# Optimization experiments

Measured on AMD Instinct MI355X. Metric: run time of the kernel, lower is better.

Reference implementation:

```python
import jax, jax.numpy as jnp
import numpy as np

B, S, E, H = 2, 2048, 1024, 16
D = E // H  # head_dim = 64


def setup_inputs() -> dict:
    key = jax.random.key(0)
    k1, k2, k3 = jax.random.split(key, 3)
    scale_in = 1.0 / np.sqrt(E)
    return {
        "x": jax.random.normal(k1, (B, S, E), dtype=jnp.float32),
        "W_attn": jax.random.normal(k2, (E, 3 * E), dtype=jnp.float32) * scale_in,
        "b_attn": jnp.zeros((3 * E,), dtype=jnp.float32),
        "W_proj": jax.random.normal(k3, (E, E), dtype=jnp.float32) * scale_in,
        "b_proj": jnp.zeros((E,), dtype=jnp.float32),
    }


def reference(x, W_attn, b_attn, W_proj, b_proj):
    # c_attn: fused QKV projection  [B,S,E] -> [B,S,3E]
    qkv = x @ W_attn + b_attn
    q, k, v = jnp.split(qkv, 3, axis=-1)
    # split heads -> [B,S,H,D]
    q = q.reshape(B, S, H, D)
    k = k.reshape(B, S, H, D)
    v = v.reshape(B, S, H, D)
    # scaled dot-product attention (no causal mask in the source module)
    scores = jnp.einsum("bqhd,bkhd->bhqk", q, k) / jnp.sqrt(jnp.float32(D))
    attn = jax.nn.softmax(scores, axis=-1)  # attn_dropout is identity in eval
    y = jnp.einsum("bhqk,bkhd->bqhd", attn, v).reshape(B, S, E)
    # c_proj; resid_dropout is identity in eval
    return y @ W_proj + b_proj
```

## Files before the change

kernel.cpp:

```cpp
#include <hip/hip_runtime.h>
#include <stdint.h>

#define NB 2
#define NS 2048
#define NE 1024
#define NH 16
#define ND 64
#define NE3 3072
#define NBS 4096
#define NT 32

typedef _Float16 half8 __attribute__((ext_vector_type(8)));
typedef __fp16 fp16x2 __attribute__((ext_vector_type(2)));
typedef float f32x4 __attribute__((ext_vector_type(4)));
typedef float f32x16 __attribute__((ext_vector_type(16)));
typedef unsigned int u32;

__device__ __forceinline__ void gload16(const void* g, void* l) {
  __builtin_amdgcn_global_load_lds(
      (__attribute__((address_space(1))) void*)const_cast<void*>(g),
      (__attribute__((address_space(3))) void*)l, 16, 0, 0);
}

__global__ void k_cvt16(const float* __restrict__ src, _Float16* __restrict__ dst, int n8) {
  int i = blockIdx.x * blockDim.x + threadIdx.x;
  if (i >= n8) return;
  const float4* s = (const float4*)src + (size_t)i * 2;
  float4 a = s[0], b = s[1];
  half8 o;
  o[0]=(_Float16)a.x; o[1]=(_Float16)a.y; o[2]=(_Float16)a.z; o[3]=(_Float16)a.w;
  o[4]=(_Float16)b.x; o[5]=(_Float16)b.y; o[6]=(_Float16)b.z; o[7]=(_Float16)b.w;
  *((half8*)dst + i) = o;
}

__global__ void k_cvtT(const float* __restrict__ src, _Float16* __restrict__ dst, int K, int N) {
  __shared__ _Float16 tile[64][72];
  int n0 = blockIdx.x * 64, k0 = blockIdx.y * 64;
  int t = threadIdx.x;
  int kk = t >> 2, nc = (t & 3) << 4;
  const float* sp = src + (size_t)(k0 + kk) * N + n0 + nc;
#pragma unroll
  for (int j = 0; j < 16; j += 4) {
    float4 v = *(const float4*)(sp + j);
    tile[kk][nc + j + 0] = (_Float16)v.x;
    tile[kk][nc + j + 1] = (_Float16)v.y;
    tile[kk][nc + j + 2] = (_Float16)v.z;
    tile[kk][nc + j + 3] = (_Float16)v.w;
  }
  __syncthreads();
  int nn = t >> 2, kc = (t & 3) << 4;
  half8 o0, o1;
#pragma unroll
  for (int j = 0; j < 8; ++j) { o0[j] = tile[kc + j][nn]; o1[j] = tile[kc + 8 + j][nn]; }
  _Float16* op = dst + (size_t)(n0 + nn) * K + k0 + kc;
  *(half8*)op = o0;
  *(half8*)(op + 8) = o1;
}

template <int OUT_HALF>
__global__ __launch_bounds__(256, 2)
void k_gemm(const _Float16* __restrict__ A, const _Float16* __restrict__ Bt,
            const float* __restrict__ bias, void* __restrict__ Cv,
            int M, int N, int K) {
  __shared__ _Float16 As[128 * 32];
  __shared__ _Float16 Bs[128 * 32];
  const int nwg = gridDim.x * gridDim.y;
  const int d = blockIdx.y * gridDim.x + blockIdx.x;
  const int lid = (d & 7) * (nwg >> 3) + (d >> 3);
  const int bx = lid % gridDim.x, by = lid / gridDim.x;
  const int m0 = by * 128, n0 = bx * 128;
  const int t = threadIdx.x, l = t & 63, w = t >> 6;
  const int wr = w >> 1, wc = w & 1;
  const int srow = l >> 2;
  const int sk = (l & 3) << 3;
  f32x4 acc[4][4] = {};
  for (int kt = 0; kt < K; kt += 32) {
    __syncthreads();
#pragma unroll
    for (int i = 0; i < 2; ++i) {
      int rb = (i * 4 + w) * 16;
      gload16(A + (size_t)(m0 + rb + srow) * K + kt + sk, (char*)As + (i * 4 + w) * 1024);
      gload16(Bt + (size_t)(n0 + rb + srow) * K + kt + sk, (char*)Bs + (i * 4 + w) * 1024);
    }
    __syncthreads();
    half8 a[4], b[4];
#pragma unroll
    for (int i = 0; i < 4; ++i)
      a[i] = *(const half8*)(As + (wr * 64 + i * 16 + (l & 15)) * 32 + ((l >> 4) << 3));
#pragma unroll
    for (int j = 0; j < 4; ++j)
      b[j] = *(const half8*)(Bs + (wc * 64 + j * 16 + (l & 15)) * 32 + ((l >> 4) << 3));
#pragma unroll
    for (int i = 0; i < 4; ++i)
#pragma unroll
      for (int j = 0; j < 4; ++j)
        acc[i][j] = __builtin_amdgcn_mfma_f32_16x16x32_f16(a[i], b[j], acc[i][j], 0, 0, 0);
  }
  float bv[4];
#pragma unroll
  for (int j = 0; j < 4; ++j) bv[j] = bias[n0 + wc * 64 + j * 16 + (l & 15)];
#pragma unroll
  for (int i = 0; i < 4; ++i) {
    int row0 = m0 + wr * 64 + i * 16 + ((l >> 4) << 2);
#pragma unroll
    for (int j = 0; j < 4; ++j) {
      int col = n0 + wc * 64 + j * 16 + (l & 15);
#pragma unroll
      for (int r = 0; r < 4; ++r) {
        float v = acc[i][j][r] + bv[j];
        if (OUT_HALF && col < NE) v *= 0.18033688011112042f;
        if (OUT_HALF)
          ((_Float16*)Cv)[(size_t)(row0 + r) * N + col] = (_Float16)v;
        else
          ((float*)Cv)[(size_t)(row0 + r) * N + col] = v;
      }
    }
  }
}

__global__ void k_vt(const _Float16* __restrict__ qkv, _Float16* __restrict__ Vt) {
  __shared__ _Float16 tile[64][72];
  int s0 = blockIdx.x * 64;
  int bh = blockIdx.y, b = bh >> 4, h = bh & 15;
  int t = threadIdx.x;
  int ss = t >> 2, dc = (t & 3) << 4;
  const _Float16* sp = qkv + (size_t)(b * NS + s0 + ss) * NE3 + 2 * NE + h * ND + dc;
  half8 v0 = *(const half8*)sp, v1 = *(const half8*)(sp + 8);
#pragma unroll
  for (int j = 0; j < 8; ++j) { tile[ss][dc + j] = v0[j]; tile[ss][dc + 8 + j] = v1[j]; }
  __syncthreads();
  int d = t >> 2, sc = (t & 3) << 4;
  half8 o0, o1;
#pragma unroll
  for (int j = 0; j < 8; ++j) { o0[j] = tile[sc + j][d]; o1[j] = tile[sc + 8 + j][d]; }
  _Float16* op = Vt + (size_t)(bh * ND + d) * NS + s0 + sc;
  *(half8*)op = o0;
  *(half8*)(op + 8) = o1;
}

__global__ __launch_bounds__(256, 2)
void k_attn(const _Float16* __restrict__ qkv, const _Float16* __restrict__ Vt,
            _Float16* __restrict__ Y) {
  __shared__ _Float16 Kb[2][64 * 64];
  __shared__ _Float16 Vb[2][64 * 64];
  const int dly = blockIdx.y * gridDim.x + blockIdx.x;
  const int lid = (dly & 7) * 64 + (dly >> 3);
  const int bh = lid >> 4, qb = lid & 15;
  const int q0 = qb * 128;
  const int b = bh >> 4, h = bh & 15;
  const int t = threadIdx.x, l = t & 63, w = t >> 6;
  const int c = l & 31, hh = l >> 5;

  half8 qf[4];
  {
    const _Float16* qp = qkv + (size_t)(b * NS + q0 + w * 32 + c) * NE3 + h * ND + 8 * hh;
    qf[0] = *(const half8*)(qp);
    qf[1] = *(const half8*)(qp + 16);
    qf[2] = *(const half8*)(qp + 32);
    qf[3] = *(const half8*)(qp + 48);
  }

  f32x16 Oa0 = {}, Oa1 = {}, Osum = {};
  f32x16 saE0, saE1, saO0, saO1;
  half8 ones;
#pragma unroll
  for (int j = 0; j < 8; ++j) ones[j] = (_Float16)1.0f;

  const int lh4 = l >> 4;
  const int ls7 = (l >> 1) & 7;
  const int l1 = l & 1;
  const int grp = c >> 1;
  const int xr = grp & 7;

#define RD_BASE (grp * 256 + ((c & 1) << 4))

#define STAGE_K(KT, BUF)                                                             \
  {                                                                                  \
    _Pragma("unroll")                                                                \
    for (int i = 0; i < 2; ++i) {                                                    \
      int ci = w * 2 + i;                                                            \
      int g = 4 * ci + lh4;                                                          \
      int row = 2 * g + l1;                                                          \
      int j8 = (ls7 ^ (g & 7)) << 3;                                                 \
      gload16(qkv + (size_t)(b * NS + (KT) * 64 + row) * NE3 + NE + h * ND + j8,     \
              (char*)&Kb[BUF][0] + ci * 1024);                                       \
    }                                                                                \
  }
#define STAGE_V(KT, BUF)                                                             \
  {                                                                                  \
    _Pragma("unroll")                                                                \
    for (int i = 0; i < 2; ++i) {                                                    \
      int ci = w * 2 + i;                                                            \
      int g = 4 * ci + lh4;                                                          \
      int row = 2 * g + l1;                                                          \
      int j8 = (ls7 ^ (g & 7)) << 3;                                                 \
      gload16(Vt + (size_t)(bh * ND + row) * NS + (KT) * 64 + j8,                    \
              (char*)&Vb[BUF][0] + ci * 1024);                                       \
    }                                                                                \
  }

#define QK_TILE(BUF, SA0, SA1)                                                       \
  {                                                                                  \
    SA0 = (f32x16){}; SA1 = (f32x16){};                                              \
    _Pragma("unroll")                                                                \
    for (int tt = 0; tt < 4; ++tt) {                                                 \
      int off = RD_BASE + (((2 * tt + hh) ^ xr) << 5);                               \
      half8 kf0 = *(const half8*)((char*)&Kb[BUF][0] + off);                         \
      half8 kf1 = *(const half8*)((char*)&Kb[BUF][0] + off + 4096);                  \
      SA0 = __builtin_amdgcn_mfma_f32_32x32x16_f16(kf0, qf[tt], SA0, 0, 0, 0);       \
      SA1 = __builtin_amdgcn_mfma_f32_32x32x16_f16(kf1, qf[tt], SA1, 0, 0, 0);       \
    }                                                                                \
  }

#define PVSTEP(KK, DARR, CUR)                                                         \
    {                                                                                 \
      u32 pb0 = DARR[2 * ((KK) & 1)][0], pa0 = DARR[2 * ((KK) & 1) + 1][0];           \
      u32 pb1 = DARR[2 * ((KK) & 1)][1], pa1 = DARR[2 * ((KK) & 1) + 1][1];           \
      u32 sent0 = hh ? pb0 : pa0;                                                     \
      u32 sent1 = hh ? pb1 : pa1;                                                     \
      u32 recv0 = __shfl_xor(sent0, 32);                                              \
      u32 recv1 = __shfl_xor(sent1, 32);                                              \
      union { u32 d[4]; half8 h; } pfu;                                               \
      pfu.d[0] = hh ? recv0 : pb0;                                                    \
      pfu.d[1] = hh ? recv1 : pb1;                                                    \
      pfu.d[2] = hh ? pa0 : recv0;                                                    \
      pfu.d[3] = hh ? pa1 : recv1;                                                    \
      int offv = RD_BASE + (((2 * (KK) + hh) ^ xr) << 5);                             \
      half8 vf0 = *(const half8*)((char*)&Vb[CUR][0] + offv);                         \
      half8 vf1 = *(const half8*)((char*)&Vb[CUR][0] + offv + 4096);                  \
      Oa0 = __builtin_amdgcn_mfma_f32_32x32x16_f16(pfu.h, vf0, Oa0, 0, 0, 0);         \
      Oa1 = __builtin_amdgcn_mfma_f32_32x32x16_f16(pfu.h, vf1, Oa1, 0, 0, 0);         \
      Osum = __builtin_amdgcn_mfma_f32_32x32x16_f16(pfu.h, ones, Osum, 0, 0, 0);      \
    }

#define TILE_BODY(T, CUR, SAC0, SAC1, SAN0, SAN1)                                     \
  {                                                                                   \
    u32 D0[4][2], D1[4][2];                                                           \
    _Pragma("unroll")                                                                 \
    for (int s = 0; s < 4; ++s) {                                                     \
      fp16x2 e0 = __builtin_amdgcn_cvt_pkrtz(__builtin_amdgcn_exp2f(SAC0[4 * s + 0]), \
                                             __builtin_amdgcn_exp2f(SAC0[4 * s + 1]));\
      fp16x2 e1 = __builtin_amdgcn_cvt_pkrtz(__builtin_amdgcn_exp2f(SAC0[4 * s + 2]), \
                                             __builtin_amdgcn_exp2f(SAC0[4 * s + 3]));\
      fp16x2 e2 = __builtin_amdgcn_cvt_pkrtz(__builtin_amdgcn_exp2f(SAC1[4 * s + 0]), \
                                             __builtin_amdgcn_exp2f(SAC1[4 * s + 1]));\
      fp16x2 e3 = __builtin_amdgcn_cvt_pkrtz(__builtin_amdgcn_exp2f(SAC1[4 * s + 2]), \
                                             __builtin_amdgcn_exp2f(SAC1[4 * s + 3]));\
      D0[s][0] = __builtin_bit_cast(u32, e0);                                         \
      D0[s][1] = __builtin_bit_cast(u32, e1);                                         \
      D1[s][0] = __builtin_bit_cast(u32, e2);                                         \
      D1[s][1] = __builtin_bit_cast(u32, e3);                                         \
    }                                                                                 \
    if ((T) + 1 < NT) QK_TILE((CUR) ^ 1, SAN0, SAN1);                                 \
    PVSTEP(0, D0, CUR)                                                                \
    PVSTEP(1, D0, CUR)                                                                \
    PVSTEP(2, D1, CUR)                                                                \
    PVSTEP(3, D1, CUR)                                                                \
    __syncthreads();                                                                  \
    if ((T) + 2 < NT) STAGE_V((T) + 2, CUR);                                          \
    if ((T) + 3 < NT) STAGE_K((T) + 3, (CUR) ^ 1);                                    \
  }

  STAGE_K(0, 0);
  STAGE_V(0, 0);
  STAGE_K(1, 1);
  __syncthreads();
  QK_TILE(0, saE0, saE1);
  __syncthreads();
  STAGE_V(1, 1);
  STAGE_K(2, 0);

  for (int kt = 0; kt < NT; kt += 2) {
    TILE_BODY(kt, 0, saE0, saE1, saO0, saO1);
    TILE_BODY(kt + 1, 1, saO0, saO1, saE0, saE1);
  }
#undef TILE_BODY
#undef PVSTEP
#undef QK_TILE
#undef STAGE_K
#undef STAGE_V
#undef RD_BASE

#pragma unroll
  for (int i = 0; i < 16; ++i) {
    int ql = (i & 3) + 8 * (i >> 2) + 4 * hh;
    float inv = 1.0f / Osum[i];
    size_t base = (size_t)(b * NS + q0 + w * 32 + ql) * NE + h * ND + c;
    Y[base] = (_Float16)(Oa0[i] * inv);
    Y[base + 32] = (_Float16)(Oa1[i] * inv);
  }
}

extern "C" void kernel_launch(void* const* d_in, const int* in_sizes, int n_in,
                              void* d_out, int out_size, void* d_ws, size_t ws_size,
                              hipStream_t stream) {
  (void)in_sizes; (void)n_in; (void)out_size; (void)ws_size;
  const float* x      = (const float*)d_in[0];
  const float* W_attn = (const float*)d_in[1];
  const float* b_attn = (const float*)d_in[2];
  const float* W_proj = (const float*)d_in[3];
  const float* b_proj = (const float*)d_in[4];
  char* ws = (char*)d_ws;
  const size_t MB = 1024 * 1024;
  _Float16* qkvb = (_Float16*)(ws);
  _Float16* WaT  = (_Float16*)(ws + 24 * MB);
  _Float16* WpT  = (_Float16*)(ws + 30 * MB);
  _Float16* xb   = (_Float16*)(ws + 32 * MB);
  _Float16* Vt   = (_Float16*)(ws + 40 * MB);
  _Float16* yb   = (_Float16*)(ws + 32 * MB);

  k_cvt16<<<dim3(2048), dim3(256), 0, stream>>>(x, xb, NBS * NE / 8);
  k_cvtT<<<dim3(48, 16), dim3(256), 0, stream>>>(W_attn, WaT, NE, NE3);
  k_cvtT<<<dim3(16, 16), dim3(256), 0, stream>>>(W_proj, WpT, NE, NE);
  k_gemm<1><<<dim3(NE3 / 128, NBS / 128), dim3(256), 0, stream>>>(xb, WaT, b_attn, (void*)qkvb, NBS, NE3, NE);
  k_vt<<<dim3(NS / 64, NB * NH), dim3(256), 0, stream>>>(qkvb, Vt);
  k_attn<<<dim3(NS / 128, NB * NH), dim3(256), 0, stream>>>(qkvb, Vt, yb);
  k_gemm<0><<<dim3(NE / 128, NBS / 128), dim3(256), 0, stream>>>(yb, WpT, b_proj, d_out, NBS, NE, NE);
}
```

Baseline: 129.2 us.

## Fuse V transpose into QKV GEMM epilogue and raise MFMA wave priority

The QKV GEMM epilogue now writes the V columns straight into the transposed Vt layout, so the separate k_vt transpose kernel and its launch are removed. In the attention kernel, s_setprio brackets the MFMA sequences to favour matrix-issuing waves. The transposed stores are strided per element, roughly 4 KB apart for adjacent rows, so they coalesce poorly and may slow the GEMM epilogue.

```diff
diff --git a/kernel.cpp b/kernel.cpp
--- a/kernel.cpp
+++ b/kernel.cpp
@@ -61,7 +61,7 @@
 __global__ __launch_bounds__(256, 2)
 void k_gemm(const _Float16* __restrict__ A, const _Float16* __restrict__ Bt,
             const float* __restrict__ bias, void* __restrict__ Cv,
-            int M, int N, int K) {
+            _Float16* __restrict__ VtOut, int M, int N, int K) {
   __shared__ _Float16 As[128 * 32];
   __shared__ _Float16 Bs[128 * 32];
   const int nwg = gridDim.x * gridDim.y;
@@ -108,34 +108,22 @@
 #pragma unroll
       for (int r = 0; r < 4; ++r) {
         float v = acc[i][j][r] + bv[j];
-        if (OUT_HALF && col < NE) v *= 0.18033688011112042f;
-        if (OUT_HALF)
-          ((_Float16*)Cv)[(size_t)(row0 + r) * N + col] = (_Float16)v;
-        else
-          ((float*)Cv)[(size_t)(row0 + r) * N + col] = v;
+        int row = row0 + r;
+        if (OUT_HALF) {
+          if (col < NE) v *= 0.18033688011112042f;
+          if (col >= 2 * NE) {
+            int vcol = col - 2 * NE;
+            int bb = row >> 11, ss = row & (NS - 1);
+            VtOut[(size_t)((bb << 10) + vcol) * NS + ss] = (_Float16)v;
+          } else {
+            ((_Float16*)Cv)[(size_t)row * N + col] = (_Float16)v;
+          }
+        } else {
+          ((float*)Cv)[(size_t)row * N + col] = v;
+        }
       }
     }
   }
-}
-
-__global__ void k_vt(const _Float16* __restrict__ qkv, _Float16* __restrict__ Vt) {
-  __shared__ _Float16 tile[64][72];
-  int s0 = blockIdx.x * 64;
-  int bh = blockIdx.y, b = bh >> 4, h = bh & 15;
-  int t = threadIdx.x;
-  int ss = t >> 2, dc = (t & 3) << 4;
-  const _Float16* sp = qkv + (size_t)(b * NS + s0 + ss) * NE3 + 2 * NE + h * ND + dc;
-  half8 v0 = *(const half8*)sp, v1 = *(const half8*)(sp + 8);
-#pragma unroll
-  for (int j = 0; j < 8; ++j) { tile[ss][dc + j] = v0[j]; tile[ss][dc + 8 + j] = v1[j]; }
-  __syncthreads();
-  int d = t >> 2, sc = (t & 3) << 4;
-  half8 o0, o1;
-#pragma unroll
-  for (int j = 0; j < 8; ++j) { o0[j] = tile[sc + j][d]; o1[j] = tile[sc + 8 + j][d]; }
-  _Float16* op = Vt + (size_t)(bh * ND + d) * NS + s0 + sc;
-  *(half8*)op = o0;
-  *(half8*)(op + 8) = o1;
 }
 
 __global__ __launch_bounds__(256, 2)
@@ -202,6 +190,7 @@
 #define QK_TILE(BUF, SA0, SA1)                                                       \
   {                                                                                  \
     SA0 = (f32x16){}; SA1 = (f32x16){};                                              \
+    __builtin_amdgcn_s_setprio(1);                                                   \
     _Pragma("unroll")                                                                \
     for (int tt = 0; tt < 4; ++tt) {                                                 \
       int off = RD_BASE + (((2 * tt + hh) ^ xr) << 5);                               \
@@ -210,6 +199,7 @@
       SA0 = __builtin_amdgcn_mfma_f32_32x32x16_f16(kf0, qf[tt], SA0, 0, 0, 0);       \
       SA1 = __builtin_amdgcn_mfma_f32_32x32x16_f16(kf1, qf[tt], SA1, 0, 0, 0);       \
     }                                                                                \
+    __builtin_amdgcn_s_setprio(0);                                                   \
   }
 
 #define PVSTEP(KK, DARR, CUR)                                                         \
@@ -228,9 +218,11 @@
       int offv = RD_BASE + (((2 * (KK) + hh) ^ xr) << 5);                             \
       half8 vf0 = *(const half8*)((char*)&Vb[CUR][0] + offv);                         \
       half8 vf1 = *(const half8*)((char*)&Vb[CUR][0] + offv + 4096);                  \
+      __builtin_amdgcn_s_setprio(1);                                                  \
       Oa0 = __builtin_amdgcn_mfma_f32_32x32x16_f16(pfu.h, vf0, Oa0, 0, 0, 0);         \
       Oa1 = __builtin_amdgcn_mfma_f32_32x32x16_f16(pfu.h, vf1, Oa1, 0, 0, 0);         \
       Osum = __builtin_amdgcn_mfma_f32_32x32x16_f16(pfu.h, ones, Osum, 0, 0, 0);      \
+      __builtin_amdgcn_s_setprio(0);                                                  \
     }
 
 #define TILE_BODY(T, CUR, SAC0, SAC1, SAN0, SAN1)                                     \
@@ -312,8 +304,7 @@
   k_cvt16<<<dim3(2048), dim3(256), 0, stream>>>(x, xb, NBS * NE / 8);
   k_cvtT<<<dim3(48, 16), dim3(256), 0, stream>>>(W_attn, WaT, NE, NE3);
   k_cvtT<<<dim3(16, 16), dim3(256), 0, stream>>>(W_proj, WpT, NE, NE);
-  k_gemm<1><<<dim3(NE3 / 128, NBS / 128), dim3(256), 0, stream>>>(xb, WaT, b_attn, (void*)qkvb, NBS, NE3, NE);
-  k_vt<<<dim3(NS / 64, NB * NH), dim3(256), 0, stream>>>(qkvb, Vt);
+  k_gemm<1><<<dim3(NE3 / 128, NBS / 128), dim3(256), 0, stream>>>(xb, WaT, b_attn, (void*)qkvb, Vt, NBS, NE3, NE);
   k_attn<<<dim3(NS / 128, NB * NH), dim3(256), 0, stream>>>(qkvb, Vt, yb);
-  k_gemm<0><<<dim3(NE / 128, NBS / 128), dim3(256), 0, stream>>>(yb, WpT, b_proj, d_out, NBS, NE, NE);
-}
+  k_gemm<0><<<dim3(NE / 128, NBS / 128), dim3(256), 0, stream>>>(yb, WpT, b_proj, d_out, nullptr, NBS, NE, NE);
+}
```

New measurement: 130.4 us. No clear change (+0.9%).

## Double-buffer GEMM LDS loads, shrink proj GEMM tile, merge weight transposes

Applied to the files above, without the earlier changes.

The GEMM kernel now double-buffers its LDS tiles. It issues the global-to-LDS loads for the stage two ahead and waits with explicit vmcnt counters, so memory latency overlaps the MFMA work instead of stalling behind two barriers per K step. The output projection GEMM uses a 64-row tile, doubling its block count to about 512 for better CU occupancy. The two weight-transpose kernels are merged into a single launch. Doubled LDS use per block may reduce occupancy, and the hand-written waitcnt values must match the number of loads in flight.

```diff
diff --git a/kernel.cpp b/kernel.cpp
--- a/kernel.cpp
+++ b/kernel.cpp
@@ -33,9 +33,15 @@
   *((half8*)dst + i) = o;
 }
 
-__global__ void k_cvtT(const float* __restrict__ src, _Float16* __restrict__ dst, int K, int N) {
+__global__ void k_cvtT2(const float* __restrict__ srcA, _Float16* __restrict__ dstA,
+                        const float* __restrict__ srcB, _Float16* __restrict__ dstB) {
   __shared__ _Float16 tile[64][72];
-  int n0 = blockIdx.x * 64, k0 = blockIdx.y * 64;
+  int bx = blockIdx.x;
+  const float* src; _Float16* dst; int N;
+  if (bx < 48) { src = srcA; dst = dstA; N = NE3; }
+  else         { src = srcB; dst = dstB; N = NE; bx -= 48; }
+  const int K = NE;
+  int n0 = bx * 64, k0 = blockIdx.y * 64;
   int t = threadIdx.x;
   int kk = t >> 2, nc = (t & 3) << 4;
   const float* sp = src + (size_t)(k0 + kk) * N + n0 + nc;
@@ -57,62 +63,96 @@
   *(half8*)(op + 8) = o1;
 }
 
-template <int OUT_HALF>
+template <int OUT_HALF, int BM>
 __global__ __launch_bounds__(256, 2)
 void k_gemm(const _Float16* __restrict__ A, const _Float16* __restrict__ Bt,
             const float* __restrict__ bias, void* __restrict__ Cv,
             int M, int N, int K) {
-  __shared__ _Float16 As[128 * 32];
-  __shared__ _Float16 Bs[128 * 32];
+  constexpr int ACH = BM / 16;
+  constexpr int CHUNKS = ACH + 8;
+  constexpr int PER_WAVE = CHUNKS / 4;
+  constexpr int JN = (BM == 128) ? 4 : 2;
+  __shared__ _Float16 As[2][BM * 32];
+  __shared__ _Float16 Bs[2][128 * 32];
   const int nwg = gridDim.x * gridDim.y;
   const int d = blockIdx.y * gridDim.x + blockIdx.x;
   const int lid = (d & 7) * (nwg >> 3) + (d >> 3);
   const int bx = lid % gridDim.x, by = lid / gridDim.x;
-  const int m0 = by * 128, n0 = bx * 128;
+  const int m0 = by * BM, n0 = bx * 128;
   const int t = threadIdx.x, l = t & 63, w = t >> 6;
-  const int wr = w >> 1, wc = w & 1;
+  const int wr = (BM == 128) ? (w >> 1) : 0;
+  const int wc = (BM == 128) ? (w & 1) : w;
   const int srow = l >> 2;
   const int sk = (l & 3) << 3;
-  f32x4 acc[4][4] = {};
-  for (int kt = 0; kt < K; kt += 32) {
-    __syncthreads();
-#pragma unroll
-    for (int i = 0; i < 2; ++i) {
-      int rb = (i * 4 + w) * 16;
-      gload16(A + (size_t)(m0 + rb + srow) * K + kt + sk, (char*)As + (i * 4 + w) * 1024);
-      gload16(Bt + (size_t)(n0 + rb + srow) * K + kt + sk, (char*)Bs + (i * 4 + w) * 1024);
+  f32x4 acc[4][JN] = {};
+
+#define G_STAGE(KT, BUF)                                                              \
+  {                                                                                   \
+    _Pragma("unroll")                                                                 \
+    for (int p = 0; p < PER_WAVE; ++p) {                                              \
+      int cid = w * PER_WAVE + p;                                                     \
+      if (cid < ACH)                                                                  \
+        gload16(A + (size_t)(m0 + cid * 16 + srow) * K + (KT) * 32 + sk,              \
+                (char*)&As[BUF][0] + cid * 1024);                                     \
+      else                                                                            \
+        gload16(Bt + (size_t)(n0 + (cid - ACH) * 16 + srow) * K + (KT) * 32 + sk,     \
+                (char*)&Bs[BUF][0] + (cid - ACH) * 1024);                             \
+    }                                                                                 \
+  }
+
+  const int T = K / 32;
+  G_STAGE(0, 0);
+  G_STAGE(1, 1);
+  for (int tt = 0; tt < T; ++tt) {
+    if (tt + 1 < T) {
+      if constexpr (PER_WAVE == 4) asm volatile("s_waitcnt vmcnt(4)" ::: "memory");
+      else                         asm volatile("s_waitcnt vmcnt(3)" ::: "memory");
+    } else {
+      asm volatile("s_waitcnt vmcnt(0)" ::: "memory");
     }
-    __syncthreads();
-    half8 a[4], b[4];
+    __builtin_amdgcn_s_barrier();
+    asm volatile("" ::: "memory");
+    const int cur = tt & 1;
+    const _Float16* as = &As[cur][0];
+    const _Float16* bs = &Bs[cur][0];
+    half8 a[4], b[JN];
 #pragma unroll
     for (int i = 0; i < 4; ++i)
-      a[i] = *(const half8*)(As + (wr * 64 + i * 16 + (l & 15)) * 32 + ((l >> 4) << 3));
-#pragma unroll
-    for (int j = 0; j < 4; ++j)
-      b[j] = *(const half8*)(Bs + (wc * 64 + j * 16 + (l & 15)) * 32 + ((l >> 4) << 3));
+      a[i] = *(const half8*)(as + (wr * 64 + i * 16 + (l & 15)) * 32 + ((l >> 4) << 3));
+#pragma unroll
+    for (int j = 0; j < JN; ++j)
+      b[j] = *(const half8*)(bs + ((BM == 128 ? wc * 64 : wc * 32) + j * 16 + (l & 15)) * 32 + ((l >> 4) << 3));
 #pragma unroll
     for (int i = 0; i < 4; ++i)
 #pragma unroll
-      for (int j = 0; j < 4; ++j)
+      for (int j = 0; j < JN; ++j)
         acc[i][j] = __builtin_amdgcn_mfma_f32_16x16x32_f16(a[i], b[j], acc[i][j], 0, 0, 0);
-  }
-  float bv[4];
-#pragma unroll
-  for (int j = 0; j < 4; ++j) bv[j] = bias[n0 + wc * 64 + j * 16 + (l & 15)];
+    asm volatile("s_waitcnt lgkmcnt(0)" ::: "memory");
+    __builtin_amdgcn_s_barrier();
+    asm volatile("" ::: "memory");
+    if (tt + 2 < T) G_STAGE(tt + 2, cur);
+  }
+#undef G_STAGE
+
+  float bv[JN];
+#pragma unroll
+  for (int j = 0; j < JN; ++j)
+    bv[j] = bias[n0 + (BM == 128 ? wc * 64 : wc * 32) + j * 16 + (l & 15)];
 #pragma unroll
   for (int i = 0; i < 4; ++i) {
     int row0 = m0 + wr * 64 + i * 16 + ((l >> 4) << 2);
 #pragma unroll
-    for (int j = 0; j < 4; ++j) {
-      int col = n0 + wc * 64 + j * 16 + (l & 15);
+    for (int j = 0; j < JN; ++j) {
+      int col = n0 + (BM == 128 ? wc * 64 : wc * 32) + j * 16 + (l & 15);
 #pragma unroll
       for (int r = 0; r < 4; ++r) {
         float v = acc[i][j][r] + bv[j];
-        if (OUT_HALF && col < NE) v *= 0.18033688011112042f;
-        if (OUT_HALF)
+        if (OUT_HALF) {
+          if (col < NE) v *= 0.18033688011112042f;
           ((_Float16*)Cv)[(size_t)(row0 + r) * N + col] = (_Float16)v;
-        else
+        } else {
           ((float*)Cv)[(size_t)(row0 + r) * N + col] = v;
+        }
       }
     }
   }
@@ -310,10 +350,9 @@
   _Float16* yb   = (_Float16*)(ws + 32 * MB);
 
   k_cvt16<<<dim3(2048), dim3(256), 0, stream>>>(x, xb, NBS * NE / 8);
-  k_cvtT<<<dim3(48, 16), dim3(256), 0, stream>>>(W_attn, WaT, NE, NE3);
-  k_cvtT<<<dim3(16, 16), dim3(256), 0, stream>>>(W_proj, WpT, NE, NE);
-  k_gemm<1><<<dim3(NE3 / 128, NBS / 128), dim3(256), 0, stream>>>(xb, WaT, b_attn, (void*)qkvb, NBS, NE3, NE);
+  k_cvtT2<<<dim3(64, 16), dim3(256), 0, stream>>>(W_attn, WaT, W_proj, WpT);
+  k_gemm<1, 128><<<dim3(NE3 / 128, NBS / 128), dim3(256), 0, stream>>>(xb, WaT, b_attn, (void*)qkvb, NBS, NE3, NE);
   k_vt<<<dim3(NS / 64, NB * NH), dim3(256), 0, stream>>>(qkvb, Vt);
   k_attn<<<dim3(NS / 128, NB * NH), dim3(256), 0, stream>>>(qkvb, Vt, yb);
-  k_gemm<0><<<dim3(NE / 128, NBS / 128), dim3(256), 0, stream>>>(yb, WpT, b_proj, d_out, NBS, NE, NE);
-}
+  k_gemm<0, 64><<<dim3(NE / 128, NBS / 64), dim3(256), 0, stream>>>(yb, WpT, b_proj, d_out, NBS, NE, NE);
+}
```

Result: faster. 126.0 us (-2.5%).
